# Performance work log

Hardware: AMD Instinct MI355X
Metric: run time of the kernel (lower is better)

Reference implementation:

```python
import jax, jax.numpy as jnp
import numpy as np

E = 16        # n_routed_experts
K = 2         # n_activated_experts (top-k)
DIM = 1024    # model dim
INTER = 704   # moe_inter_dim
B, S = 4, 1024


def setup_inputs() -> dict:
    key = jax.random.key(0)
    ks = jax.random.split(key, 5)
    x = jax.random.normal(ks[0], (B, S, DIM), dtype=jnp.float32)
    Wg = jax.random.normal(ks[1], (E, DIM), dtype=jnp.float32) * 0.02   # gate (Linear, no bias)
    W1 = jax.random.normal(ks[2], (E, DIM, INTER), dtype=jnp.float32) * 0.02
    W3 = jax.random.normal(ks[3], (E, DIM, INTER), dtype=jnp.float32) * 0.02
    W2 = jax.random.normal(ks[4], (E, INTER, DIM), dtype=jnp.float32) * 0.02
    return {"x": x, "Wg": Wg, "W1": W1, "W2": W2, "W3": W3}


def reference(x, Wg, W1, W2, W3):
    # Single-process semantics of MoEWithAll2All: the all2all dispatch/combine is
    # pure communication; the math is: softmax router -> top-k -> renormalize ->
    # per-expert SwiGLU MLP on routed tokens -> weighted combine at original slots.
    Bb, Ss, D = x.shape
    xf = x.reshape(-1, D)                              # [N, D], N = B*S
    logits = xf @ Wg.T                                 # [N, E]
    probs = jax.nn.softmax(logits, axis=-1)
    topw, topi = jax.lax.top_k(probs, K)               # [N, K]
    topw = topw / topw.sum(axis=-1, keepdims=True)
    # gates[n, e] = routed weight of token n for expert e (0 if not routed):
    # identical math to the masked gather/scatter dispatch in the original.
    gates = (jax.nn.one_hot(topi, E, dtype=xf.dtype) * topw[..., None]).sum(axis=1)  # [N, E]
    out = jnp.zeros_like(xf)
    for e in range(E):                                 # small fixed loop over experts
        h = jax.nn.silu(xf @ W1[e]) * (xf @ W3[e])     # SwiGLU expert, [N, INTER]
        out = out + gates[:, e:e + 1] * (h @ W2[e])    # combine with gate weights
    return out.reshape(Bb, Ss, D)
```

## Files before the change

### kernel.cpp

```cpp
#include <hip/hip_runtime.h>

#define NTOK 4096
#define DDIM 1024
#define IDIM 704
#define NEXP 16
#define NSLOT 8192
#define MAXT 128
#define NPAD1 768
#define RTRBLK 512
#define TRBLK 2240

typedef __attribute__((ext_vector_type(8))) short bf16x8;
typedef __attribute__((ext_vector_type(4))) float f32x4;
typedef __attribute__((ext_vector_type(4))) unsigned short us4;
typedef __attribute__((ext_vector_type(8))) unsigned short us8;

__device__ __forceinline__ unsigned short f2bf(float f) {
  union { float f; unsigned int u; } v; v.f = f;
  unsigned int r = v.u + 0x7fffu + ((v.u >> 16) & 1u);
  return (unsigned short)(r >> 16);
}

__device__ __forceinline__ float bf2f(unsigned short b) {
  union { unsigned int u; float f; } v; v.u = ((unsigned int)b) << 16;
  return v.f;
}

__device__ __forceinline__ void gload_lds16(const void* g, void* l) {
  __builtin_amdgcn_global_load_lds((const __attribute__((address_space(1))) void*)g,
                                   (__attribute__((address_space(3))) void*)l, 16, 0, 0);
}

__global__ __launch_bounds__(256, 4)
void k_front(const float* __restrict__ x, const float* __restrict__ Wg,
             const float* __restrict__ W1, const float* __restrict__ W3,
             const float* __restrict__ W2, int* __restrict__ tok_e,
             float* __restrict__ tok_w, unsigned short* __restrict__ Xb,
             unsigned short* __restrict__ W1T, unsigned short* __restrict__ W3T,
             unsigned short* __restrict__ W2T) {
  int b = blockIdx.x;
  if (b >= RTRBLK) {
    __shared__ unsigned short lds[4][64 * 64];
    int tb = b - RTRBLK;
    const float* src; unsigned short* dst;
    int ksz, nsz, kx, np, e;
    if (tb < 1536) {
      int which = tb >= 768 ? 1 : 0;
      int t2 = tb - which * 768;
      kx = t2 & 15; int rest = t2 >> 4; np = rest % 3; e = rest / 3;
      ksz = DDIM; nsz = IDIM;
      src = (which ? W3 : W1) + (size_t)e * DDIM * IDIM;
      dst = (which ? W3T : W1T) + (size_t)e * NPAD1 * DDIM;
    } else {
      int t3 = tb - 1536;
      kx = t3 % 11; int rest = t3 / 11; np = rest & 3; e = rest >> 2;
      ksz = IDIM; nsz = DDIM;
      src = W2 + (size_t)e * IDIM * DDIM;
      dst = W2T + (size_t)e * DDIM * IDIM;
    }
    int k0 = kx * 64, n0 = np * 256;
    int t = threadIdx.x;
    int kr4 = (t >> 4) * 4, nc4 = (t & 15) * 4;
    f32x4 v[4][4];
    bool val[4];
#pragma unroll
    for (int s = 0; s < 4; ++s) {
      val[s] = (n0 + s * 64 + 64) <= nsz;
      if (val[s]) {
#pragma unroll
        for (int j = 0; j < 4; ++j)
          v[s][j] = *(const f32x4*)(src + (size_t)(k0 + kr4 + j) * nsz + n0 + s * 64 + nc4);
      }
    }
    int c8 = kr4 >> 3, half = (kr4 >> 2) & 1;
#pragma unroll
    for (int s = 0; s < 4; ++s) {
      if (val[s]) {
#pragma unroll
        for (int i = 0; i < 4; ++i) {
          int row = nc4 + i;
          int addr = row * 64 + ((c8 ^ ((row >> 2) & 7)) << 3) + half * 4;
          us4 o;
#pragma unroll
          for (int j = 0; j < 4; ++j) o[j] = f2bf(v[s][j][i]);
          *(us4*)(lds[s] + addr) = o;
        }
      }
    }
    __syncthreads();
    int nr = t >> 3, kc8 = t & 7;
#pragma unroll
    for (int s = 0; s < 4; ++s) {
#pragma unroll
      for (int q = 0; q < 2; ++q) {
        int row = nr + q * 32;
        us8 o = val[s] ? *(const us8*)(lds[s] + row * 64 + ((kc8 ^ ((row >> 2) & 7)) << 3))
                       : (us8)(unsigned short)0;
        *(us8*)(dst + (size_t)(n0 + s * 64 + row) * ksz + k0 + kc8 * 8) = o;
      }
    }
    return;
  }
  int lane = threadIdx.x & 63;
  int wv = threadIdx.x >> 6;
  int tk0 = b * 8 + wv * 2;
  f32x4 xv[2][4];
#pragma unroll
  for (int tok = 0; tok < 2; ++tok) {
    const f32x4* xr = (const f32x4*)(x + (size_t)(tk0 + tok) * DDIM);
    us4* xbr = (us4*)(Xb + (size_t)(tk0 + tok) * DDIM);
#pragma unroll
    for (int c = 0; c < 4; ++c) {
      xv[tok][c] = xr[c * 64 + lane];
      us4 o;
#pragma unroll
      for (int j = 0; j < 4; ++j) o[j] = f2bf(xv[tok][c][j]);
      xbr[c * 64 + lane] = o;
    }
  }
  float p[2][NEXP];
#pragma unroll
  for (int e = 0; e < NEXP; ++e) {
    const f32x4* wr = (const f32x4*)(Wg + (size_t)e * DDIM);
    float s0 = 0.f, s1 = 0.f;
#pragma unroll
    for (int c = 0; c < 4; ++c) {
      f32x4 w4 = wr[c * 64 + lane];
      s0 += xv[0][c][0]*w4[0] + xv[0][c][1]*w4[1] + xv[0][c][2]*w4[2] + xv[0][c][3]*w4[3];
      s1 += xv[1][c][0]*w4[0] + xv[1][c][1]*w4[1] + xv[1][c][2]*w4[2] + xv[1][c][3]*w4[3];
    }
    p[0][e] = s0; p[1][e] = s1;
  }
#pragma unroll
  for (int off = 32; off >= 1; off >>= 1)
#pragma unroll
    for (int e = 0; e < NEXP; ++e) {
      p[0][e] += __shfl_xor(p[0][e], off);
      p[1][e] += __shfl_xor(p[1][e], off);
    }
#pragma unroll
  for (int tok = 0; tok < 2; ++tok) {
    int i0 = 0; float b0 = p[tok][0];
#pragma unroll
    for (int e = 1; e < NEXP; ++e) if (p[tok][e] > b0) { b0 = p[tok][e]; i0 = e; }
    int i1 = -1; float b1 = -3.4e38f;
#pragma unroll
    for (int e = 0; e < NEXP; ++e) if (e != i0 && p[tok][e] > b1) { b1 = p[tok][e]; i1 = e; }
    if (lane == 0) {
      int tk = tk0 + tok;
      float w0 = 1.f / (1.f + __expf(b1 - b0));
      tok_e[2*tk] = i0; tok_e[2*tk+1] = i1;
      tok_w[2*tk] = w0; tok_w[2*tk+1] = 1.f - w0;
    }
  }
}

__global__ void k_scan_scatter(const int* __restrict__ tok_e, const float* __restrict__ tok_w,
                               int* __restrict__ counts, int* __restrict__ offsets,
                               int* __restrict__ ntiles, int* __restrict__ tile_e,
                               int* __restrict__ tile_m0, int* __restrict__ token_map,
                               float* __restrict__ gate_w, int* __restrict__ slot_of) {
  int eb = blockIdx.x;
  int t = threadIdx.x, lane = t & 63, wv = t >> 6;
  __shared__ unsigned long long masks[4][32];
  __shared__ int wcnt[4][NEXP];
  __shared__ int counts_s[NEXP];
  int ce[NEXP];
#pragma unroll
  for (int e = 0; e < NEXP; ++e) ce[e] = 0;
  int base = wv * 2048 + lane;
  int te = tok_e[base];
#pragma unroll 1
  for (int s = 0; s < 32; ++s) {
    int ten = (s < 31) ? tok_e[base + (s + 1) * 64] : 0;
    unsigned long long B0 = __ballot(te & 1);
    unsigned long long B1 = __ballot(te & 2);
    unsigned long long B2 = __ballot(te & 4);
    unsigned long long B3 = __ballot(te & 8);
#pragma unroll
    for (int e = 0; e < NEXP; ++e) {
      unsigned long long m = ((e & 1) ? B0 : ~B0) & ((e & 2) ? B1 : ~B1) &
                             ((e & 4) ? B2 : ~B2) & ((e & 8) ? B3 : ~B3);
      ce[e] += (int)__popcll(m);
      if (e == eb && lane == 0) masks[wv][s] = m;
    }
    te = ten;
  }
  if (lane == 0) {
#pragma unroll
    for (int e = 0; e < NEXP; ++e) wcnt[wv][e] = ce[e];
  }
  __syncthreads();
  if (t < NEXP) {
    int s = wcnt[0][t] + wcnt[1][t] + wcnt[2][t] + wcnt[3][t];
    counts_s[t] = s;
    if (eb == 0) counts[t] = s;
  }
  __syncthreads();
  if (eb == 0 && t == 0) {
    int acc = 0, nt = 0;
    for (int e = 0; e < NEXP; ++e) {
      offsets[e] = acc;
      int cc = counts_s[e];
      for (int m0 = 0; m0 < cc; m0 += 128) { tile_e[nt] = e; tile_m0[nt] = m0; ++nt; }
      acc += cc;
    }
    offsets[NEXP] = acc;
    *ntiles = nt;
  }
  int run = 0;
  for (int e = 0; e < eb; ++e) run += counts_s[e];
  for (int w = 0; w < wv; ++w) run += wcnt[w][eb];
  unsigned long long below = (lane == 63) ? 0x7fffffffffffffffull : ((1ull << lane) - 1ull);
#pragma unroll 1
  for (int s = 0; s < 32; ++s) {
    unsigned long long m = masks[wv][s];
    if ((m >> lane) & 1ull) {
      int i = wv * 2048 + s * 64 + lane;
      int slot = run + (int)__popcll(m & below);
      token_map[slot] = i >> 1;
      gate_w[slot] = tok_w[i];
      slot_of[i] = slot;
    }
    run += (int)__popcll(m);
  }
}

__global__ __launch_bounds__(256, 2)
void k_gemm1(const unsigned short* __restrict__ Xb, const unsigned short* __restrict__ W1T,
             const unsigned short* __restrict__ W3T, const int* __restrict__ token_map,
             const float* __restrict__ gate_w, const int* __restrict__ ntiles,
             const int* __restrict__ tile_e, const int* __restrict__ tile_m0,
             const int* __restrict__ offsets, const int* __restrict__ counts,
             unsigned short* __restrict__ H) {
  int idx = blockIdx.x;
  int xcd = idx & 7, r = idx >> 3;
  int g = (r >> 2) * 8 + xcd;
  int mm = r & 3;
  int ty = (g / 6) * 4 + mm;
  if (ty >= *ntiles) return;
  int n0 = (g % 6) * 128;
  int e = tile_e[ty], m0 = tile_m0[ty];
  int base_slot = offsets[e] + m0;
  int cnt = counts[e] - m0; if (cnt > 128) cnt = 128;

  __shared__ unsigned short As[2][128 * 32];
  __shared__ unsigned short B1s[2][128 * 32];
  __shared__ unsigned short B3s[2][128 * 32];

  int t = threadIdx.x;
  int row = t >> 2, kc = (t & 3) * 8;
  int r0i = base_slot + row;      if (r0i > NSLOT - 1) r0i = NSLOT - 1;
  int r1i = base_slot + 64 + row; if (r1i > NSLOT - 1) r1i = NSLOT - 1;
  const unsigned short* ag0 = Xb + (size_t)token_map[r0i] * DDIM + kc;
  const unsigned short* ag1 = Xb + (size_t)token_map[r1i] * DDIM + kc;
  const unsigned short* b1g0 = W1T + ((size_t)e * NPAD1 + n0 + row) * DDIM + kc;
  const unsigned short* b1g1 = b1g0 + (size_t)64 * DDIM;
  const unsigned short* b3g0 = W3T + ((size_t)e * NPAD1 + n0 + row) * DDIM + kc;
  const unsigned short* b3g1 = b3g0 + (size_t)64 * DDIM;
  int d0 = t * 8, d1 = 2048 + t * 8;

  int lane = t & 63, wv = t >> 6;
  int wm = (wv >> 1) * 64, wn = (wv & 1) * 64;
  int lm = lane & 15, kg = lane >> 4;
  int ao[4], bo[4];
#pragma unroll
  for (int i = 0; i < 4; ++i) {
    ao[i] = (wm + i * 16 + lm) * 32 + kg * 8;
    bo[i] = (wn + i * 16 + lm) * 32 + kg * 8;
  }

  f32x4 acc1[4][4], acc3[4][4];
#pragma unroll
  for (int i = 0; i < 4; ++i)
#pragma unroll
    for (int j = 0; j < 4; ++j) { acc1[i][j] = 0.f; acc3[i][j] = 0.f; }

  gload_lds16(ag0, As[0] + d0);
  gload_lds16(ag1, As[0] + d1);
  gload_lds16(b1g0, B1s[0] + d0);
  gload_lds16(b1g1, B1s[0] + d1);
  gload_lds16(b3g0, B3s[0] + d0);
  gload_lds16(b3g1, B3s[0] + d1);

  for (int k0 = 0; k0 < DDIM; k0 += 32) {
    int cur = (k0 >> 5) & 1;
    __syncthreads();
    if (k0 + 32 < DDIM) {
      int nx = cur ^ 1, kn = k0 + 32;
      gload_lds16(ag0 + kn, As[nx] + d0);
      gload_lds16(ag1 + kn, As[nx] + d1);
      gload_lds16(b1g0 + kn, B1s[nx] + d0);
      gload_lds16(b1g1 + kn, B1s[nx] + d1);
      gload_lds16(b3g0 + kn, B3s[nx] + d0);
      gload_lds16(b3g1 + kn, B3s[nx] + d1);
    }
    bf16x8 av[4], b1v[4], b3v[4];
#pragma unroll
    for (int i = 0; i < 4; ++i) {
      av[i]  = *(const bf16x8*)(As[cur] + ao[i]);
      b1v[i] = *(const bf16x8*)(B1s[cur] + bo[i]);
      b3v[i] = *(const bf16x8*)(B3s[cur] + bo[i]);
    }
#pragma unroll
    for (int mi = 0; mi < 4; ++mi)
#pragma unroll
      for (int ni = 0; ni < 4; ++ni) {
        acc1[mi][ni] = __builtin_amdgcn_mfma_f32_16x16x32_bf16(av[mi], b1v[ni], acc1[mi][ni], 0, 0, 0);
        acc3[mi][ni] = __builtin_amdgcn_mfma_f32_16x16x32_bf16(av[mi], b3v[ni], acc3[mi][ni], 0, 0, 0);
      }
  }

#pragma unroll
  for (int mi = 0; mi < 4; ++mi)
#pragma unroll
    for (int rr = 0; rr < 4; ++rr) {
      int orow = wm + mi * 16 + kg * 4 + rr;
      if (orow < cnt) {
        int slot = base_slot + orow;
        float gw = gate_w[slot];
        unsigned short* hrow = H + (size_t)slot * IDIM;
#pragma unroll
        for (int ni = 0; ni < 4; ++ni) {
          int nn = n0 + wn + ni * 16 + lm;
          if (nn < IDIM) {
            float v1 = acc1[mi][ni][rr];
            float v3 = acc3[mi][ni][rr];
            float hh = v1 / (1.f + __expf(-v1)) * v3 * gw;
            hrow[nn] = f2bf(hh);
          }
        }
      }
    }
}

__global__ __launch_bounds__(256, 3)
void k_gemm2(const unsigned short* __restrict__ H, const unsigned short* __restrict__ W2T,
             const int* __restrict__ ntiles, const int* __restrict__ tile_e,
             const int* __restrict__ tile_m0, const int* __restrict__ offsets,
             const int* __restrict__ counts, unsigned short* __restrict__ O2) {
  int idx = blockIdx.x;
  int xcd = idx & 7, r = idx >> 3;
  int g = (r >> 2) * 8 + xcd;
  int mm = r & 3;
  int ty = (g >> 3) * 4 + mm;
  if (ty >= *ntiles) return;
  int n0 = (g & 7) * 128;
  int e = tile_e[ty], m0 = tile_m0[ty];
  int base_slot = offsets[e] + m0;
  int cnt = counts[e] - m0; if (cnt > 128) cnt = 128;

  __shared__ unsigned short As[2][128 * 32];
  __shared__ unsigned short Bs[2][128 * 32];

  int t = threadIdx.x;
  int row = t >> 2, kc = (t & 3) * 8;
  int r0i = base_slot + row;      if (r0i > NSLOT - 1) r0i = NSLOT - 1;
  int r1i = base_slot + 64 + row; if (r1i > NSLOT - 1) r1i = NSLOT - 1;
  const unsigned short* ag0 = H + (size_t)r0i * IDIM + kc;
  const unsigned short* ag1 = H + (size_t)r1i * IDIM + kc;
  const unsigned short* bg0 = W2T + ((size_t)e * DDIM + n0 + row) * IDIM + kc;
  const unsigned short* bg1 = bg0 + (size_t)64 * IDIM;
  int d0 = t * 8, d1 = 2048 + t * 8;

  int lane = t & 63, wv = t >> 6;
  int wm = (wv >> 1) * 64, wn = (wv & 1) * 64;
  int lm = lane & 15, kg = lane >> 4;
  int ao[4], bo[4];
#pragma unroll
  for (int i = 0; i < 4; ++i) {
    ao[i] = (wm + i * 16 + lm) * 32 + kg * 8;
    bo[i] = (wn + i * 16 + lm) * 32 + kg * 8;
  }

  f32x4 acc[4][4];
#pragma unroll
  for (int i = 0; i < 4; ++i)
#pragma unroll
    for (int j = 0; j < 4; ++j) acc[i][j] = 0.f;

  gload_lds16(ag0, As[0] + d0);
  gload_lds16(ag1, As[0] + d1);
  gload_lds16(bg0, Bs[0] + d0);
  gload_lds16(bg1, Bs[0] + d1);

  for (int k0 = 0; k0 < IDIM; k0 += 32) {
    int cur = (k0 >> 5) & 1;
    __syncthreads();
    if (k0 + 32 < IDIM) {
      int nx = cur ^ 1, kn = k0 + 32;
      gload_lds16(ag0 + kn, As[nx] + d0);
      gload_lds16(ag1 + kn, As[nx] + d1);
      gload_lds16(bg0 + kn, Bs[nx] + d0);
      gload_lds16(bg1 + kn, Bs[nx] + d1);
    }
    bf16x8 av[4], bv[4];
#pragma unroll
    for (int i = 0; i < 4; ++i) {
      av[i] = *(const bf16x8*)(As[cur] + ao[i]);
      bv[i] = *(const bf16x8*)(Bs[cur] + bo[i]);
    }
#pragma unroll
    for (int mi = 0; mi < 4; ++mi)
#pragma unroll
      for (int ni = 0; ni < 4; ++ni)
        acc[mi][ni] = __builtin_amdgcn_mfma_f32_16x16x32_bf16(av[mi], bv[ni], acc[mi][ni], 0, 0, 0);
  }

#pragma unroll
  for (int mi = 0; mi < 4; ++mi)
#pragma unroll
    for (int rr = 0; rr < 4; ++rr) {
      int orow = wm + mi * 16 + kg * 4 + rr;
      if (orow < cnt) {
        unsigned short* op = O2 + (size_t)(base_slot + orow) * DDIM + n0;
#pragma unroll
        for (int ni = 0; ni < 4; ++ni)
          op[wn + ni * 16 + lm] = f2bf(acc[mi][ni][rr]);
      }
    }
}

__global__ void k_combine(const unsigned short* __restrict__ O2, const int* __restrict__ slot_of,
                          float* __restrict__ out) {
  int tk = blockIdx.x, tt = threadIdx.x;
  int s0 = slot_of[2 * tk], s1 = slot_of[2 * tk + 1];
  us4 a = ((const us4*)(O2 + (size_t)s0 * DDIM))[tt];
  us4 b = ((const us4*)(O2 + (size_t)s1 * DDIM))[tt];
  f32x4 o;
#pragma unroll
  for (int j = 0; j < 4; ++j) o[j] = bf2f(a[j]) + bf2f(b[j]);
  ((f32x4*)(out + (size_t)tk * DDIM))[tt] = o;
}

extern "C" void kernel_launch(void* const* d_in, const int* in_sizes, int n_in,
                              void* d_out, int out_size, void* d_ws, size_t ws_size,
                              hipStream_t stream) {
  const float* x  = (const float*)d_in[0];
  const float* Wg = (const float*)d_in[1];
  const float* W1 = (const float*)d_in[2];
  const float* W2 = (const float*)d_in[3];
  const float* W3 = (const float*)d_in[4];
  float* out = (float*)d_out;

  char* ws = (char*)d_ws;
  size_t off = 0;
  unsigned short* Xb = (unsigned short*)(ws + off); off += (size_t)NTOK * DDIM * 2;
  unsigned short* H  = (unsigned short*)(ws + off); off += (size_t)NSLOT * IDIM * 2;
  unsigned short* O2 = (unsigned short*)(ws + off); off += (size_t)NSLOT * DDIM * 2;
  unsigned short* W1T = (unsigned short*)(ws + off); off += (size_t)NEXP * NPAD1 * DDIM * 2;
  unsigned short* W3T = (unsigned short*)(ws + off); off += (size_t)NEXP * NPAD1 * DDIM * 2;
  unsigned short* W2T = (unsigned short*)(ws + off); off += (size_t)NEXP * DDIM * IDIM * 2;
  int* counts  = (int*)(ws + off); off += 64;
  int* offsets = (int*)(ws + off); off += 128;
  int* ntiles  = (int*)(ws + off); off += 64;
  int* tile_e  = (int*)(ws + off); off += MAXT * 4;
  int* tile_m0 = (int*)(ws + off); off += MAXT * 4;
  int* tok_e   = (int*)(ws + off); off += NSLOT * 4;
  float* tok_w = (float*)(ws + off); off += NSLOT * 4;
  int* token_map = (int*)(ws + off); off += NSLOT * 4;
  float* gate_w  = (float*)(ws + off); off += NSLOT * 4;
  int* slot_of   = (int*)(ws + off); off += NSLOT * 4;

  k_front<<<RTRBLK + TRBLK, 256, 0, stream>>>(x, Wg, W1, W3, W2, tok_e, tok_w, Xb,
                                              W1T, W3T, W2T);
  k_scan_scatter<<<NEXP, 256, 0, stream>>>(tok_e, tok_w, counts, offsets, ntiles,
                                           tile_e, tile_m0, token_map, gate_w, slot_of);
  k_gemm1<<<480, 256, 0, stream>>>(Xb, W1T, W3T, token_map, gate_w, ntiles, tile_e,
                                   tile_m0, offsets, counts, H);
  k_gemm2<<<640, 256, 0, stream>>>(H, W2T, ntiles, tile_e, tile_m0, offsets, counts, O2);
  k_combine<<<4096, 256, 0, stream>>>(O2, slot_of, out);
}
```

Before: 305.5 us.

## Use larger 256x128 transpose tiles for weight bf16 conversion blocks

Restructures the weight transpose/convert blocks in the front kernel to process 256(K)x128(N) tiles through a 64KB LDS buffer with a rotation swizzle, instead of 64x256 tiles in four 64x64 sub-buffers. Each thread now writes full 512-byte rows, so global stores become longer contiguous runs, and the transpose block count drops accordingly. In exchange, LDS use per block grows and launch bounds are relaxed to 2 blocks per SM, which lowers occupancy for the router blocks that share this kernel.

```diff
diff --git a/kernel.cpp b/kernel.cpp
--- a/kernel.cpp
+++ b/kernel.cpp
@@ -8,7 +8,7 @@
 #define MAXT 128
 #define NPAD1 768
 #define RTRBLK 512
-#define TRBLK 2240
+#define TRBLK 1152
 
 typedef __attribute__((ext_vector_type(8))) short bf16x8;
 typedef __attribute__((ext_vector_type(4))) float f32x4;
@@ -31,7 +31,7 @@
                                    (__attribute__((address_space(3))) void*)l, 16, 0, 0);
 }
 
-__global__ __launch_bounds__(256, 4)
+__global__ __launch_bounds__(256, 2)
 void k_front(const float* __restrict__ x, const float* __restrict__ Wg,
              const float* __restrict__ W1, const float* __restrict__ W3,
              const float* __restrict__ W2, int* __restrict__ tok_e,
@@ -40,64 +40,73 @@
              unsigned short* __restrict__ W2T) {
   int b = blockIdx.x;
   if (b >= RTRBLK) {
-    __shared__ unsigned short lds[4][64 * 64];
+    __shared__ char ldsb[128 * 512];
     int tb = b - RTRBLK;
     const float* src; unsigned short* dst;
-    int ksz, nsz, kx, np, e;
-    if (tb < 1536) {
-      int which = tb >= 768 ? 1 : 0;
-      int t2 = tb - which * 768;
-      kx = t2 & 15; int rest = t2 >> 4; np = rest % 3; e = rest / 3;
-      ksz = DDIM; nsz = IDIM;
+    int KS, NS, k0, n0;
+    if (tb < 768) {
+      int which = tb >= 384 ? 1 : 0;
+      int t2 = tb - which * 384;
+      int e = t2 / 24, rem = t2 % 24;
+      int kb = rem / 6, nb = rem % 6;
+      KS = DDIM; NS = IDIM;
+      k0 = kb * 256; n0 = nb * 128;
       src = (which ? W3 : W1) + (size_t)e * DDIM * IDIM;
       dst = (which ? W3T : W1T) + (size_t)e * NPAD1 * DDIM;
     } else {
-      int t3 = tb - 1536;
-      kx = t3 % 11; int rest = t3 / 11; np = rest & 3; e = rest >> 2;
-      ksz = IDIM; nsz = DDIM;
+      int t2 = tb - 768;
+      int e = t2 / 24, rem = t2 % 24;
+      int kb = rem / 8, nb = rem % 8;
+      KS = IDIM; NS = DDIM;
+      k0 = kb * 256; n0 = nb * 128;
       src = W2 + (size_t)e * IDIM * DDIM;
       dst = W2T + (size_t)e * DDIM * IDIM;
     }
-    int k0 = kx * 64, n0 = np * 256;
     int t = threadIdx.x;
-    int kr4 = (t >> 4) * 4, nc4 = (t & 15) * 4;
-    f32x4 v[4][4];
-    bool val[4];
-#pragma unroll
-    for (int s = 0; s < 4; ++s) {
-      val[s] = (n0 + s * 64 + 64) <= nsz;
-      if (val[s]) {
-#pragma unroll
-        for (int j = 0; j < 4; ++j)
-          v[s][j] = *(const f32x4*)(src + (size_t)(k0 + kr4 + j) * nsz + n0 + s * 64 + nc4);
-      }
-    }
-    int c8 = kr4 >> 3, half = (kr4 >> 2) & 1;
-#pragma unroll
-    for (int s = 0; s < 4; ++s) {
-      if (val[s]) {
-#pragma unroll
-        for (int i = 0; i < 4; ++i) {
-          int row = nc4 + i;
-          int addr = row * 64 + ((c8 ^ ((row >> 2) & 7)) << 3) + half * 4;
-          us4 o;
-#pragma unroll
-          for (int j = 0; j < 4; ++j) o[j] = f2bf(v[s][j][i]);
-          *(us4*)(lds[s] + addr) = o;
+    int l = t & 31;
+    int g8 = t >> 5;
+    int n4 = l * 4;
+    int nn = n0 + n4;
+    bool nok = (nn + 4) <= NS;
+#pragma unroll
+    for (int h = 0; h < 2; ++h) {
+      f32x4 v[4][4];
+#pragma unroll
+      for (int i = 0; i < 4; ++i) {
+        int kl0 = (h * 4 + i) * 32 + g8 * 4;
+#pragma unroll
+        for (int j = 0; j < 4; ++j) {
+          int kk = k0 + kl0 + j;
+          bool ok = nok && (kk < KS);
+          v[i][j] = ok ? *(const f32x4*)(src + (size_t)kk * NS + nn) : (f32x4)0.f;
         }
       }
+#pragma unroll
+      for (int i = 0; i < 4; ++i) {
+        int kl0 = (h * 4 + i) * 32 + g8 * 4;
+        int chunk0 = kl0 >> 3;
+        int off8 = (kl0 * 2) & 15;
+        int phys = (chunk0 + l) & 31;
+#pragma unroll
+        for (int c = 0; c < 4; ++c) {
+          int row = n4 + c;
+          us4 o = { f2bf(v[i][0][c]), f2bf(v[i][1][c]), f2bf(v[i][2][c]), f2bf(v[i][3][c]) };
+          *(us4*)(ldsb + row * 512 + phys * 16 + off8) = o;
+        }
+      }
     }
     __syncthreads();
-    int nr = t >> 3, kc8 = t & 7;
-#pragma unroll
-    for (int s = 0; s < 4; ++s) {
-#pragma unroll
-      for (int q = 0; q < 2; ++q) {
-        int row = nr + q * 32;
-        us8 o = val[s] ? *(const us8*)(lds[s] + row * 64 + ((kc8 ^ ((row >> 2) & 7)) << 3))
-                       : (us8)(unsigned short)0;
-        *(us8*)(dst + (size_t)(n0 + s * 64 + row) * ksz + k0 + kc8 * 8) = o;
-      }
+    int cl = t & 31;
+    int rg = t >> 5;
+    int kk = k0 + cl * 8;
+    bool kok = kk < KS;
+#pragma unroll
+    for (int r = 0; r < 16; ++r) {
+      int row = r * 8 + rg;
+      int phys = (cl + (row >> 2)) & 31;
+      us8 o = *(const us8*)(ldsb + row * 512 + phys * 16);
+      if (kok)
+        *(us8*)(dst + (size_t)(n0 + row) * KS + kk) = o;
     }
     return;
   }
```

After: 303.8 us. Within noise of the previous version (-0.6%).

## Fuse weight fp32-to-bf16 transpose into GEMM B-tile loads, drop pre-pass

Applied to the files above, without the earlier changes.

The separate pre-pass that transposed and converted W1/W3/W2 to bf16 in workspace is removed. The GEMM kernels now load fp32 weights straight into registers, convert them with packed bf16 conversion instructions and write them into a swizzled LDS layout after the MFMA step of each iteration. This removes a full read-write pass over all expert weights. In exchange, each weight tile is re-read in fp32 (twice the bytes) by every M-tile that uses the same expert, and the register-staged prefetch replaces the async global-to-LDS loads.

```diff
diff --git a/kernel.cpp b/kernel.cpp
--- a/kernel.cpp
+++ b/kernel.cpp
@@ -6,14 +6,12 @@
 #define NEXP 16
 #define NSLOT 8192
 #define MAXT 128
-#define NPAD1 768
 #define RTRBLK 512
-#define TRBLK 2240
 
 typedef __attribute__((ext_vector_type(8))) short bf16x8;
 typedef __attribute__((ext_vector_type(4))) float f32x4;
 typedef __attribute__((ext_vector_type(4))) unsigned short us4;
-typedef __attribute__((ext_vector_type(8))) unsigned short us8;
+typedef __attribute__((ext_vector_type(2))) unsigned int u32x2;
 
 __device__ __forceinline__ unsigned short f2bf(float f) {
   union { float f; unsigned int u; } v; v.f = f;
@@ -26,81 +24,39 @@
   return v.f;
 }
 
+__device__ __forceinline__ unsigned int cvt_pk_bf16(float a, float b) {
+  unsigned int r;
+  asm("v_cvt_pk_bf16_f32 %0, %1, %2" : "=v"(r) : "v"(a), "v"(b));
+  return r;
+}
+
 __device__ __forceinline__ void gload_lds16(const void* g, void* l) {
   __builtin_amdgcn_global_load_lds((const __attribute__((address_space(1))) void*)g,
                                    (__attribute__((address_space(3))) void*)l, 16, 0, 0);
 }
 
+__device__ __forceinline__ void load_b(const float* wt, int ns, bool ok, f32x4* v) {
+#pragma unroll
+  for (int j = 0; j < 4; ++j)
+    v[j] = ok ? *(const f32x4*)(wt + (size_t)j * ns) : (f32x4)0.f;
+}
+
+__device__ __forceinline__ void write_b(const f32x4* v, unsigned short* buf, int kk, int nq) {
+  int h8 = (kk & 1) * 8;
+  int phys = (kk >> 1) ^ (nq & 3);
+#pragma unroll
+  for (int c = 0; c < 4; ++c) {
+    int row = nq * 4 + c;
+    u32x2 o = { cvt_pk_bf16(v[0][c], v[1][c]), cvt_pk_bf16(v[2][c], v[3][c]) };
+    *(u32x2*)((char*)buf + row * 64 + phys * 16 + h8) = o;
+  }
+}
+
 __global__ __launch_bounds__(256, 4)
 void k_front(const float* __restrict__ x, const float* __restrict__ Wg,
-             const float* __restrict__ W1, const float* __restrict__ W3,
-             const float* __restrict__ W2, int* __restrict__ tok_e,
-             float* __restrict__ tok_w, unsigned short* __restrict__ Xb,
-             unsigned short* __restrict__ W1T, unsigned short* __restrict__ W3T,
-             unsigned short* __restrict__ W2T) {
+             int* __restrict__ tok_e, float* __restrict__ tok_w,
+             unsigned short* __restrict__ Xb) {
   int b = blockIdx.x;
-  if (b >= RTRBLK) {
-    __shared__ unsigned short lds[4][64 * 64];
-    int tb = b - RTRBLK;
-    const float* src; unsigned short* dst;
-    int ksz, nsz, kx, np, e;
-    if (tb < 1536) {
-      int which = tb >= 768 ? 1 : 0;
-      int t2 = tb - which * 768;
-      kx = t2 & 15; int rest = t2 >> 4; np = rest % 3; e = rest / 3;
-      ksz = DDIM; nsz = IDIM;
-      src = (which ? W3 : W1) + (size_t)e * DDIM * IDIM;
-      dst = (which ? W3T : W1T) + (size_t)e * NPAD1 * DDIM;
-    } else {
-      int t3 = tb - 1536;
-      kx = t3 % 11; int rest = t3 / 11; np = rest & 3; e = rest >> 2;
-      ksz = IDIM; nsz = DDIM;
-      src = W2 + (size_t)e * IDIM * DDIM;
-      dst = W2T + (size_t)e * DDIM * IDIM;
-    }
-    int k0 = kx * 64, n0 = np * 256;
-    int t = threadIdx.x;
-    int kr4 = (t >> 4) * 4, nc4 = (t & 15) * 4;
-    f32x4 v[4][4];
-    bool val[4];
-#pragma unroll
-    for (int s = 0; s < 4; ++s) {
-      val[s] = (n0 + s * 64 + 64) <= nsz;
-      if (val[s]) {
-#pragma unroll
-        for (int j = 0; j < 4; ++j)
-          v[s][j] = *(const f32x4*)(src + (size_t)(k0 + kr4 + j) * nsz + n0 + s * 64 + nc4);
-      }
-    }
-    int c8 = kr4 >> 3, half = (kr4 >> 2) & 1;
-#pragma unroll
-    for (int s = 0; s < 4; ++s) {
-      if (val[s]) {
-#pragma unroll
-        for (int i = 0; i < 4; ++i) {
-          int row = nc4 + i;
-          int addr = row * 64 + ((c8 ^ ((row >> 2) & 7)) << 3) + half * 4;
-          us4 o;
-#pragma unroll
-          for (int j = 0; j < 4; ++j) o[j] = f2bf(v[s][j][i]);
-          *(us4*)(lds[s] + addr) = o;
-        }
-      }
-    }
-    __syncthreads();
-    int nr = t >> 3, kc8 = t & 7;
-#pragma unroll
-    for (int s = 0; s < 4; ++s) {
-#pragma unroll
-      for (int q = 0; q < 2; ++q) {
-        int row = nr + q * 32;
-        us8 o = val[s] ? *(const us8*)(lds[s] + row * 64 + ((kc8 ^ ((row >> 2) & 7)) << 3))
-                       : (us8)(unsigned short)0;
-        *(us8*)(dst + (size_t)(n0 + s * 64 + row) * ksz + k0 + kc8 * 8) = o;
-      }
-    }
-    return;
-  }
   int lane = threadIdx.x & 63;
   int wv = threadIdx.x >> 6;
   int tk0 = b * 8 + wv * 2;
@@ -227,8 +183,8 @@
 }
 
 __global__ __launch_bounds__(256, 2)
-void k_gemm1(const unsigned short* __restrict__ Xb, const unsigned short* __restrict__ W1T,
-             const unsigned short* __restrict__ W3T, const int* __restrict__ token_map,
+void k_gemm1(const unsigned short* __restrict__ Xb, const float* __restrict__ W1,
+             const float* __restrict__ W3, const int* __restrict__ token_map,
              const float* __restrict__ gate_w, const int* __restrict__ ntiles,
              const int* __restrict__ tile_e, const int* __restrict__ tile_m0,
              const int* __restrict__ offsets, const int* __restrict__ counts,
@@ -249,16 +205,17 @@
   __shared__ unsigned short B3s[2][128 * 32];
 
   int t = threadIdx.x;
-  int row = t >> 2, kc = (t & 3) * 8;
-  int r0i = base_slot + row;      if (r0i > NSLOT - 1) r0i = NSLOT - 1;
-  int r1i = base_slot + 64 + row; if (r1i > NSLOT - 1) r1i = NSLOT - 1;
+  int arow = t >> 2, kc = (t & 3) * 8;
+  int r0i = base_slot + arow;      if (r0i > NSLOT - 1) r0i = NSLOT - 1;
+  int r1i = base_slot + 64 + arow; if (r1i > NSLOT - 1) r1i = NSLOT - 1;
   const unsigned short* ag0 = Xb + (size_t)token_map[r0i] * DDIM + kc;
   const unsigned short* ag1 = Xb + (size_t)token_map[r1i] * DDIM + kc;
-  const unsigned short* b1g0 = W1T + ((size_t)e * NPAD1 + n0 + row) * DDIM + kc;
-  const unsigned short* b1g1 = b1g0 + (size_t)64 * DDIM;
-  const unsigned short* b3g0 = W3T + ((size_t)e * NPAD1 + n0 + row) * DDIM + kc;
-  const unsigned short* b3g1 = b3g0 + (size_t)64 * DDIM;
   int d0 = t * 8, d1 = 2048 + t * 8;
+
+  int kk = t >> 5, nq = t & 31;
+  bool bok = (n0 + nq * 4 + 4) <= IDIM;
+  const float* w1t = W1 + (size_t)e * DDIM * IDIM + (size_t)(kk * 4) * IDIM + (n0 + nq * 4);
+  const float* w3t = W3 + (size_t)e * DDIM * IDIM + (size_t)(kk * 4) * IDIM + (n0 + nq * 4);
 
   int lane = t & 63, wv = t >> 6;
   int wm = (wv >> 1) * 64, wn = (wv & 1) * 64;
@@ -267,7 +224,8 @@
 #pragma unroll
   for (int i = 0; i < 4; ++i) {
     ao[i] = (wm + i * 16 + lm) * 32 + kg * 8;
-    bo[i] = (wn + i * 16 + lm) * 32 + kg * 8;
+    int brow = wn + i * 16 + lm;
+    bo[i] = brow * 64 + ((kg ^ ((brow >> 2) & 3)) << 4);
   }
 
   f32x4 acc1[4][4], acc3[4][4];
@@ -276,31 +234,34 @@
 #pragma unroll
     for (int j = 0; j < 4; ++j) { acc1[i][j] = 0.f; acc3[i][j] = 0.f; }
 
-  gload_lds16(ag0, As[0] + d0);
-  gload_lds16(ag1, As[0] + d1);
-  gload_lds16(b1g0, B1s[0] + d0);
-  gload_lds16(b1g1, B1s[0] + d1);
-  gload_lds16(b3g0, B3s[0] + d0);
-  gload_lds16(b3g1, B3s[0] + d1);
+  {
+    gload_lds16(ag0, As[0] + d0);
+    gload_lds16(ag1, As[0] + d1);
+    f32x4 b1r[4], b3r[4];
+    load_b(w1t, IDIM, bok, b1r);
+    load_b(w3t, IDIM, bok, b3r);
+    write_b(b1r, B1s[0], kk, nq);
+    write_b(b3r, B3s[0], kk, nq);
+  }
 
   for (int k0 = 0; k0 < DDIM; k0 += 32) {
-    int cur = (k0 >> 5) & 1;
+    int cur = (k0 >> 5) & 1, nx = cur ^ 1;
     __syncthreads();
-    if (k0 + 32 < DDIM) {
-      int nx = cur ^ 1, kn = k0 + 32;
+    f32x4 b1r[4], b3r[4];
+    bool more = (k0 + 32) < DDIM;
+    if (more) {
+      int kn = k0 + 32;
       gload_lds16(ag0 + kn, As[nx] + d0);
       gload_lds16(ag1 + kn, As[nx] + d1);
-      gload_lds16(b1g0 + kn, B1s[nx] + d0);
-      gload_lds16(b1g1 + kn, B1s[nx] + d1);
-      gload_lds16(b3g0 + kn, B3s[nx] + d0);
-      gload_lds16(b3g1 + kn, B3s[nx] + d1);
+      load_b(w1t + (size_t)kn * IDIM, IDIM, bok, b1r);
+      load_b(w3t + (size_t)kn * IDIM, IDIM, bok, b3r);
     }
     bf16x8 av[4], b1v[4], b3v[4];
 #pragma unroll
     for (int i = 0; i < 4; ++i) {
       av[i]  = *(const bf16x8*)(As[cur] + ao[i]);
-      b1v[i] = *(const bf16x8*)(B1s[cur] + bo[i]);
-      b3v[i] = *(const bf16x8*)(B3s[cur] + bo[i]);
+      b1v[i] = *(const bf16x8*)((const char*)B1s[cur] + bo[i]);
+      b3v[i] = *(const bf16x8*)((const char*)B3s[cur] + bo[i]);
     }
 #pragma unroll
     for (int mi = 0; mi < 4; ++mi)
@@ -309,6 +270,10 @@
         acc1[mi][ni] = __builtin_amdgcn_mfma_f32_16x16x32_bf16(av[mi], b1v[ni], acc1[mi][ni], 0, 0, 0);
         acc3[mi][ni] = __builtin_amdgcn_mfma_f32_16x16x32_bf16(av[mi], b3v[ni], acc3[mi][ni], 0, 0, 0);
       }
+    if (more) {
+      write_b(b1r, B1s[nx], kk, nq);
+      write_b(b3r, B3s[nx], kk, nq);
+    }
   }
 
 #pragma unroll
@@ -335,7 +300,7 @@
 }
 
 __global__ __launch_bounds__(256, 3)
-void k_gemm2(const unsigned short* __restrict__ H, const unsigned short* __restrict__ W2T,
+void k_gemm2(const unsigned short* __restrict__ H, const float* __restrict__ W2,
              const int* __restrict__ ntiles, const int* __restrict__ tile_e,
              const int* __restrict__ tile_m0, const int* __restrict__ offsets,
              const int* __restrict__ counts, unsigned short* __restrict__ O2) {
@@ -354,14 +319,15 @@
   __shared__ unsigned short Bs[2][128 * 32];
 
   int t = threadIdx.x;
-  int row = t >> 2, kc = (t & 3) * 8;
-  int r0i = base_slot + row;      if (r0i > NSLOT - 1) r0i = NSLOT - 1;
-  int r1i = base_slot + 64 + row; if (r1i > NSLOT - 1) r1i = NSLOT - 1;
+  int arow = t >> 2, kc = (t & 3) * 8;
+  int r0i = base_slot + arow;      if (r0i > NSLOT - 1) r0i = NSLOT - 1;
+  int r1i = base_slot + 64 + arow; if (r1i > NSLOT - 1) r1i = NSLOT - 1;
   const unsigned short* ag0 = H + (size_t)r0i * IDIM + kc;
   const unsigned short* ag1 = H + (size_t)r1i * IDIM + kc;
-  const unsigned short* bg0 = W2T + ((size_t)e * DDIM + n0 + row) * IDIM + kc;
-  const unsigned short* bg1 = bg0 + (size_t)64 * IDIM;
   int d0 = t * 8, d1 = 2048 + t * 8;
+
+  int kk = t >> 5, nq = t & 31;
+  const float* w2t = W2 + (size_t)e * IDIM * DDIM + (size_t)(kk * 4) * DDIM + (n0 + nq * 4);
 
   int lane = t & 63, wv = t >> 6;
   int wm = (wv >> 1) * 64, wn = (wv & 1) * 64;
@@ -370,7 +336,8 @@
 #pragma unroll
   for (int i = 0; i < 4; ++i) {
     ao[i] = (wm + i * 16 + lm) * 32 + kg * 8;
-    bo[i] = (wn + i * 16 + lm) * 32 + kg * 8;
+    int brow = wn + i * 16 + lm;
+    bo[i] = brow * 64 + ((kg ^ ((brow >> 2) & 3)) << 4);
   }
 
   f32x4 acc[4][4];
@@ -379,32 +346,37 @@
 #pragma unroll
     for (int j = 0; j < 4; ++j) acc[i][j] = 0.f;
 
-  gload_lds16(ag0, As[0] + d0);
-  gload_lds16(ag1, As[0] + d1);
-  gload_lds16(bg0, Bs[0] + d0);
-  gload_lds16(bg1, Bs[0] + d1);
+  {
+    gload_lds16(ag0, As[0] + d0);
+    gload_lds16(ag1, As[0] + d1);
+    f32x4 br[4];
+    load_b(w2t, DDIM, true, br);
+    write_b(br, Bs[0], kk, nq);
+  }
 
   for (int k0 = 0; k0 < IDIM; k0 += 32) {
-    int cur = (k0 >> 5) & 1;
+    int cur = (k0 >> 5) & 1, nx = cur ^ 1;
     __syncthreads();
-    if (k0 + 32 < IDIM) {
-      int nx = cur ^ 1, kn = k0 + 32;
+    f32x4 br[4];
+    bool more = (k0 + 32) < IDIM;
+    if (more) {
+      int kn = k0 + 32;
       gload_lds16(ag0 + kn, As[nx] + d0);
       gload_lds16(ag1 + kn, As[nx] + d1);
-      gload_lds16(bg0 + kn, Bs[nx] + d0);
-      gload_lds16(bg1 + kn, Bs[nx] + d1);
+      load_b(w2t + (size_t)kn * DDIM, DDIM, true, br);
     }
     bf16x8 av[4], bv[4];
 #pragma unroll
     for (int i = 0; i < 4; ++i) {
       av[i] = *(const bf16x8*)(As[cur] + ao[i]);
-      bv[i] = *(const bf16x8*)(Bs[cur] + bo[i]);
+      bv[i] = *(const bf16x8*)((const char*)Bs[cur] + bo[i]);
     }
 #pragma unroll
     for (int mi = 0; mi < 4; ++mi)
 #pragma unroll
       for (int ni = 0; ni < 4; ++ni)
         acc[mi][ni] = __builtin_amdgcn_mfma_f32_16x16x32_bf16(av[mi], bv[ni], acc[mi][ni], 0, 0, 0);
+    if (more) write_b(br, Bs[nx], kk, nq);
   }
 
 #pragma unroll
@@ -448,9 +420,6 @@
   unsigned short* Xb = (unsigned short*)(ws + off); off += (size_t)NTOK * DDIM * 2;
   unsigned short* H  = (unsigned short*)(ws + off); off += (size_t)NSLOT * IDIM * 2;
   unsigned short* O2 = (unsigned short*)(ws + off); off += (size_t)NSLOT * DDIM * 2;
-  unsigned short* W1T = (unsigned short*)(ws + off); off += (size_t)NEXP * NPAD1 * DDIM * 2;
-  unsigned short* W3T = (unsigned short*)(ws + off); off += (size_t)NEXP * NPAD1 * DDIM * 2;
-  unsigned short* W2T = (unsigned short*)(ws + off); off += (size_t)NEXP * DDIM * IDIM * 2;
   int* counts  = (int*)(ws + off); off += 64;
   int* offsets = (int*)(ws + off); off += 128;
   int* ntiles  = (int*)(ws + off); off += 64;
@@ -462,12 +431,11 @@
   float* gate_w  = (float*)(ws + off); off += NSLOT * 4;
   int* slot_of   = (int*)(ws + off); off += NSLOT * 4;
 
-  k_front<<<RTRBLK + TRBLK, 256, 0, stream>>>(x, Wg, W1, W3, W2, tok_e, tok_w, Xb,
-                                              W1T, W3T, W2T);
+  k_front<<<RTRBLK, 256, 0, stream>>>(x, Wg, tok_e, tok_w, Xb);
   k_scan_scatter<<<NEXP, 256, 0, stream>>>(tok_e, tok_w, counts, offsets, ntiles,
                                            tile_e, tile_m0, token_map, gate_w, slot_of);
-  k_gemm1<<<480, 256, 0, stream>>>(Xb, W1T, W3T, token_map, gate_w, ntiles, tile_e,
+  k_gemm1<<<480, 256, 0, stream>>>(Xb, W1, W3, token_map, gate_w, ntiles, tile_e,
                                    tile_m0, offsets, counts, H);
-  k_gemm2<<<640, 256, 0, stream>>>(H, W2T, ntiles, tile_e, tile_m0, offsets, counts, O2);
+  k_gemm2<<<640, 256, 0, stream>>>(H, W2, ntiles, tile_e, tile_m0, offsets, counts, O2);
   k_combine<<<4096, 256, 0, stream>>>(O2, slot_of, out);
 }
```

After: 318.3 us. 1.04x slower.
